# Kernel tuning notes

Measured on AMD Instinct MI355X. Metric: run time of the kernel, lower is better.

## Reference

```python
import jax, jax.numpy as jnp
import numpy as np

GRID_SIZE, SPLINE_ORDER = 5, 3  # efficient-kan KANLinear defaults
NUM_BASES = GRID_SIZE + SPLINE_ORDER


def b_splines(x, grid):
    # x: (N, in_dim), grid: (in_dim, GRID_SIZE + 2*SPLINE_ORDER + 1)
    xe = x[..., None]
    bases = ((xe >= grid[:, :-1]) & (xe < grid[:, 1:])).astype(x.dtype)
    for k in range(1, SPLINE_ORDER + 1):  # Cox-de Boor recursion (static, 3 iters)
        left = (xe - grid[:, : -(k + 1)]) / (grid[:, k:-1] - grid[:, : -(k + 1)])
        right = (grid[:, k + 1:] - xe) / (grid[:, k + 1:] - grid[:, 1:-k])
        bases = left * bases[..., :-1] + right * bases[..., 1:]
    return bases  # (N, in_dim, NUM_BASES)


def kan_linear(x, grid, base_w, spline_w, scaler):
    # base branch: SiLU(x) @ W_base^T ; spline branch: B-spline basis @ scaled spline weights
    n = x.shape[0]
    out_dim = base_w.shape[0]
    base = jax.nn.silu(x) @ base_w.T
    bs = b_splines(x, grid).reshape(n, -1)                    # (N, in*NUM_BASES)
    sw = (spline_w * scaler[..., None]).reshape(out_dim, -1)  # (out, in*NUM_BASES)
    return base + bs @ sw.T


def setup_inputs() -> dict:
    key = jax.random.key(0)
    N, E, F, H, C, L = 50000, 500000, 128, 128, 40, 3
    ks = jax.random.split(key, 8)
    x = jax.random.normal(ks[0], (N, F), dtype=jnp.float32)
    edge_index = jax.random.randint(ks[1], (2, E), 0, N)
    # KAN grid (registered buffer in efficient-kan): uniform over [-1,1] extended by spline_order
    h_step = 2.0 / GRID_SIZE
    pts = np.arange(-SPLINE_ORDER, GRID_SIZE + SPLINE_ORDER + 1) * h_step - 1.0
    grid_mp = jnp.asarray(np.tile(pts, (F, 1)), dtype=jnp.float32)
    D = F + L * H  # skip-concat dim into output KANLinear
    grid_out = jnp.asarray(np.tile(pts, (D, 1)), dtype=jnp.float32)
    s = 0.1
    conv_base_w = jax.random.normal(ks[2], (L, H, F), dtype=jnp.float32) * s
    conv_spline_w = jax.random.normal(ks[3], (L, H, F, NUM_BASES), dtype=jnp.float32) * s
    conv_scaler = jnp.ones((L, H, F), dtype=jnp.float32)
    conv_bias = jnp.zeros((L, H), dtype=jnp.float32)
    bn_gamma = jnp.ones((L, H), dtype=jnp.float32)
    bn_beta = jnp.zeros((L, H), dtype=jnp.float32)
    out_base_w = jax.random.normal(ks[4], (C, D), dtype=jnp.float32) * s
    out_spline_w = jax.random.normal(ks[5], (C, D, NUM_BASES), dtype=jnp.float32) * s
    out_scaler = jnp.ones((C, D), dtype=jnp.float32)
    return dict(x=x, edge_index=edge_index, grid_mp=grid_mp, conv_base_w=conv_base_w,
                conv_spline_w=conv_spline_w, conv_scaler=conv_scaler, conv_bias=conv_bias,
                bn_gamma=bn_gamma, bn_beta=bn_beta, grid_out=grid_out,
                out_base_w=out_base_w, out_spline_w=out_spline_w, out_scaler=out_scaler)


def reference(x, edge_index, grid_mp, conv_base_w, conv_spline_w, conv_scaler, conv_bias,
              bn_gamma, bn_beta, grid_out, out_base_w, out_spline_w, out_scaler):
    N = x.shape[0]
    L = conv_base_w.shape[0]
    # GCN normalization with self-loops (computed once; identical each layer)
    loop = jnp.arange(N)
    src = jnp.concatenate([edge_index[0], loop])
    dst = jnp.concatenate([edge_index[1], loop])
    deg = jax.ops.segment_sum(jnp.ones_like(src, dtype=x.dtype), dst, num_segments=N)
    dinv = jnp.where(deg > 0, jax.lax.rsqrt(jnp.maximum(deg, 1.0)), 0.0)
    norm = dinv[src] * dinv[dst]  # (E+N,)
    feats = [x]
    for i in range(L):  # static layer loop
        h = kan_linear(x, grid_mp, conv_base_w[i], conv_spline_w[i], conv_scaler[i])
        # symmetric-normalized sparse aggregation (gather on src, scatter-add on dst)
        h = jax.ops.segment_sum(h[src] * norm[:, None], dst, num_segments=N) + conv_bias[i]
        # BatchNorm1d (training mode: biased batch statistics over nodes)
        mu = h.mean(axis=0)
        var = h.var(axis=0)
        x = (h - mu) * jax.lax.rsqrt(var + 1e-5) * bn_gamma[i] + bn_beta[i]
        feats.append(x)  # dropout p=0.0 is identity
    xc = jnp.concatenate(feats, axis=1)  # skip-concat: (N, F + L*H)
    logits = kan_linear(xc, grid_out, out_base_w, out_spline_w, out_scaler)
    return jax.nn.log_softmax(logits, axis=1)
```

## Files before the change

### kernel.cpp

```cpp
#include <hip/hip_runtime.h>
#include <hip/hip_bf16.h>
#include <math.h>

#define F_IN   128
#define HID    128
#define NLAYER 3
#define NCLS   40
#define DCAT   512
#define OOUT   64

typedef short s16x8 __attribute__((ext_vector_type(8)));
typedef unsigned short u16x8 __attribute__((ext_vector_type(8)));
typedef unsigned short u16x4 __attribute__((ext_vector_type(4)));
typedef float f32x4 __attribute__((ext_vector_type(4)));
typedef unsigned long long u64x2 __attribute__((ext_vector_type(2)));


static __device__ __forceinline__ float silu_f(float x) {
    return x / (1.f + __expf(-x));
}

static __device__ __forceinline__ unsigned short f2bf_rn(float f) {
    union { __hip_bfloat16 h; unsigned short u; } cv;
    cv.h = __float2bfloat16(f);
    return cv.u;
}

static __device__ __forceinline__ float bf2f(unsigned short u) {
    return __uint_as_float((unsigned)u << 16);
}

static __device__ __forceinline__ void lds_barrier() {
    asm volatile("s_waitcnt lgkmcnt(0)" ::: "memory");
    __builtin_amdgcn_s_barrier();
}


__global__ __launch_bounds__(256) void deg_init_kernel(int* deg, int N) {
    for (int i = blockIdx.x * blockDim.x + threadIdx.x; i < N; i += gridDim.x * blockDim.x)
        deg[i] = 1;
}

__global__ __launch_bounds__(256) void deg_count_kernel(const int* __restrict__ dst, int E, int* deg) {
    for (int i = blockIdx.x * blockDim.x + threadIdx.x; i < E; i += gridDim.x * blockDim.x)
        atomicAdd(&deg[dst[i]], 1);
}

__global__ __launch_bounds__(256) void dinv_kernel(const int* __restrict__ deg, float* dinv, int N) {
    for (int i = blockIdx.x * blockDim.x + threadIdx.x; i < N; i += gridDim.x * blockDim.x)
        dinv[i] = rsqrtf((float)deg[i]);
}

__global__ __launch_bounds__(256) void scan_reduce_kernel(const int* __restrict__ deg, int* __restrict__ bsum, int N) {
    __shared__ int sh[256];
    int t = threadIdx.x;
    int e = blockIdx.x * 256 + t;
    sh[t] = (e < N) ? deg[e] : 0;
    __syncthreads();
#pragma unroll
    for (int off = 128; off > 0; off >>= 1) {
        if (t < off) sh[t] += sh[t + off];
        __syncthreads();
    }
    if (t == 0) bsum[blockIdx.x] = sh[0];
}

__global__ __launch_bounds__(256) void scan_top_kernel(const int* __restrict__ bsum, int* __restrict__ bbase, int nsb) {
    __shared__ int sh[256];
    int t = threadIdx.x;
    int chunk = (nsb + 255) >> 8;
    int begin = t * chunk;
    int end = begin + chunk; if (end > nsb) end = nsb;
    int s = 0;
    for (int i = begin; i < end; ++i) s += bsum[i];
    sh[t] = s;
    __syncthreads();
#pragma unroll
    for (int off = 1; off < 256; off <<= 1) {
        int v = 0;
        if (t >= off) v = sh[t - off];
        __syncthreads();
        if (t >= off) sh[t] += v;
        __syncthreads();
    }
    int run = (t == 0) ? 0 : sh[t - 1];
    for (int i = begin; i < end; ++i) {
        bbase[i] = run;
        run += bsum[i];
    }
}

__global__ __launch_bounds__(256) void scan_write_kernel(const int* __restrict__ deg,
                                                         const int* __restrict__ bbase,
                                                         int* __restrict__ offs, int* __restrict__ cursor, int N) {
    __shared__ int sh[256];
    int t = threadIdx.x;
    int e = blockIdx.x * 256 + t;
    int d = (e < N) ? deg[e] : 0;
    sh[t] = d;
    __syncthreads();
#pragma unroll
    for (int off = 1; off < 256; off <<= 1) {
        int v = 0;
        if (t >= off) v = sh[t - off];
        __syncthreads();
        if (t >= off) sh[t] += v;
        __syncthreads();
    }
    int incl = sh[t] + bbase[blockIdx.x];
    int excl = incl - d;
    if (e < N) {
        offs[e] = excl;
        cursor[e] = excl;
        if (e == N - 1) offs[N] = incl;
    }
}

__global__ __launch_bounds__(256) void fill_kernel(const int* __restrict__ src, const int* __restrict__ dst,
                                                   int E, int N, int* cursor, int* __restrict__ csr) {
    int total = E + N;
    for (int i = blockIdx.x * blockDim.x + threadIdx.x; i < total; i += gridDim.x * blockDim.x) {
        if (i < E) {
            int d = dst[i];
            int p = atomicAdd(&cursor[d], 1);
            csr[p] = src[i];
        } else {
            int n = i - E;
            int p = atomicAdd(&cursor[n], 1);
            csr[p] = n;
        }
    }
}

__global__ __launch_bounds__(256) void pack_conv_mfma(const float* __restrict__ bw,
                                                      const float* __restrict__ sw,
                                                      const float* __restrict__ sc,
                                                      unsigned short* __restrict__ wpk) {
    int total = NLAYER * 9 * 4 * 8 * 64 * 8;
    for (int idx = blockIdx.x * blockDim.x + threadIdx.x; idx < total; idx += gridDim.x * blockDim.x) {
        int e    = idx & 7;
        int lane = (idx >> 3) & 63;
        int cf   = (idx >> 9) & 7;
        int kk   = (idx >> 12) & 3;
        int cc   = (idx >> 14) % 9;
        int l    = idx / (9 << 14);
        int o = cf * 16 + (lane & 15);
        int k = kk * 32 + ((lane >> 4) << 3) + e;
        float v;
        if (cc == 8) {
            v = bw[(l * 128 + o) * 128 + k];
        } else {
            int f = cc * 16 + (k >> 3);
            int j = k & 7;
            int base = (l * 128 + o) * 128 + f;
            v = sw[base * 8 + j] * sc[base];
        }
        wpk[idx] = f2bf_rn(v);
    }
}

__global__ __launch_bounds__(256) void pack_out_mfma(const float* __restrict__ bw,
                                                     const float* __restrict__ sw,
                                                     const float* __restrict__ sc,
                                                     unsigned short* __restrict__ wpk) {
    int total = 36 * 4 * 4 * 64 * 8;
    for (int idx = blockIdx.x * blockDim.x + threadIdx.x; idx < total; idx += gridDim.x * blockDim.x) {
        int e    = idx & 7;
        int lane = (idx >> 3) & 63;
        int cf   = (idx >> 9) & 3;
        int kk   = (idx >> 11) & 3;
        int gcc  = idx >> 13;
        int g = gcc / 9, cc = gcc % 9;
        int o = cf * 16 + (lane & 15);
        int k = kk * 32 + ((lane >> 4) << 3) + e;
        float v = 0.f;
        if (o < NCLS) {
            if (cc == 8) {
                int f = g * 128 + k;
                v = bw[o * DCAT + f];
            } else {
                int f = g * 128 + cc * 16 + (k >> 3);
                int j = k & 7;
                int base = o * DCAT + f;
                v = sw[base * 8 + j] * sc[base];
            }
        }
        wpk[idx] = f2bf_rn(v);
    }
}


__global__ __launch_bounds__(512) void affine_init_kernel(float* scA, float* shA) {
    int i = threadIdx.x;
    scA[i] = 1.f; shA[i] = 0.f;
}

template<bool CONV, bool INIT>
__global__ __launch_bounds__(256, 2) void kan_fused_kernel(
    const float* __restrict__ xin, int xstride, int in_off,
    const float* __restrict__ scA, const float* __restrict__ shA,
    const unsigned short* __restrict__ wconv,
    const unsigned short* __restrict__ wout,
    unsigned short* __restrict__ htmp,
    const float* __restrict__ dinv,
    float* __restrict__ out_acc, int N) {

    __shared__ __align__(16) char lds_phi0[16384];
    __shared__ __align__(16) char lds_phi1[16384];

    const int tid = threadIdx.x;
    const int lane = tid & 63;
    const int wave = tid >> 6;
    const int l15 = lane & 15, lg = lane >> 4;
    const int nblk = blockIdx.x * 64;

    const float g0 = -1.f - 3.f * 0.4f;
    const float invh = 1.f / 0.4f;

    const int fg = tid & 3;
    const int n0 = tid >> 2;

    f32x4 accc[4][2];
    f32x4 acco[4];
    if (CONV) {
#pragma unroll
        for (int r = 0; r < 4; ++r)
#pragma unroll
            for (int c = 0; c < 2; ++c) accc[r][c] = (f32x4)0.f;
    }
#pragma unroll
    for (int r = 0; r < 4; ++r) acco[r] = (f32x4)0.f;

    float4 xqb[2], scb[2], shb[2];
    auto ldx = [&](int cc, int slot) {
        int f0 = in_off + cc * 16 + fg * 4;
        scb[slot] = *(const float4*)(scA + f0);
        shb[slot] = *(const float4*)(shA + f0);
        int gn = nblk + n0;
        xqb[slot] = (gn < N) ? *(const float4*)(xin + (size_t)gn * xstride + f0)
                             : (float4){0.f, 0.f, 0.f, 0.f};
    };

    s16x8 wc_reg[4][2];
    s16x8 wo_reg[4];
    auto loadW = [&](int cc) {
        if (CONV) {
            const unsigned short* wcb = wconv + (size_t)cc * 16384;
#pragma unroll
            for (int kk = 0; kk < 4; ++kk)
#pragma unroll
                for (int c = 0; c < 2; ++c) {
                    int cf = wave * 2 + c;
                    wc_reg[kk][c] = *(const s16x8*)(wcb + (((size_t)kk * 8 + cf) * 64 + lane) * 8);
                }
        }
        const unsigned short* wob = wout + (size_t)cc * 8192;
#pragma unroll
        for (int kk = 0; kk < 4; ++kk)
            wo_reg[kk] = *(const s16x8*)(wob + (((size_t)kk * 4 + wave) * 64 + lane) * 8);
    };

    u16x4 sreg[8];

    u64x2 pcur[4];
    auto phi_compute = [&](int ccc, int slot) {
        float xi[4] = {xqb[slot].x, xqb[slot].y, xqb[slot].z, xqb[slot].w};
        float scr[4] = {scb[slot].x, scb[slot].y, scb[slot].z, scb[slot].w};
        float shr[4] = {shb[slot].x, shb[slot].y, shb[slot].z, shb[slot].w};
        u16x4 sv;
#pragma unroll
        for (int fl = 0; fl < 4; ++fl) {
            float y = fmaf(xi[fl], scr[fl], shr[fl]);
            sv[fl] = f2bf_rn(silu_f(y));
            float t = (y - g0) * invh;
            float cfl = floorf(t);
            int c = (int)cfl;
            c = c < -20 ? -20 : (c > 20 ? 20 : c);
            float u = t - cfl;
            float um = 1.f - u;
            float u2 = u * u;
            float um2 = um * um;
            float w0 = um2 * um * (1.f / 6.f);
            float w3 = u2 * u * (1.f / 6.f);
            float w1 = fmaf(fmaf(0.5f, u, -1.f), u2, 2.f / 3.f);
            float w2 = fmaf(fmaf(-0.5f, u, 0.5f), u2, fmaf(0.5f, u, 1.f / 6.f));
            unsigned long long W = (unsigned long long)f2bf_rn(w0)
                                 | ((unsigned long long)f2bf_rn(w1) << 16)
                                 | ((unsigned long long)f2bf_rn(w2) << 32)
                                 | ((unsigned long long)f2bf_rn(w3) << 48);
            int pos = (c - 3) * 16;
            unsigned long long lo = (pos >= 0) ? (W << (pos & 63)) : (W >> ((-pos) & 63));
            lo = (pos >= 64 || pos <= -64) ? 0ull : lo;
            int ph = pos - 64;
            unsigned long long hi = (ph >= 0) ? (W << (ph & 63)) : (W >> ((-ph) & 63));
            hi = (ph >= 64 || ph <= -64) ? 0ull : hi;
            u64x2 v; v.x = lo; v.y = hi;
            pcur[fl] = v;
        }
        sreg[ccc] = sv;
    };

    auto write_phi = [&](char* buf) {
        int swz = (n0 & 7) << 4;
#pragma unroll
        for (int i = 0; i < 4; ++i) {
            int byte = n0 * 256 + ((fg * 64 + i * 16) ^ swz);
            *(u64x2*)(buf + byte) = pcur[i];
        }
    };

    auto write_silu = [&](char* buf) {
        int swz = (n0 & 7) << 4;
#pragma unroll
        for (int ccc = 0; ccc < 8; ++ccc) {
            int byte = n0 * 256 + (((ccc * 16 + fg * 4) * 2) ^ swz);
            *(u16x4*)(buf + byte) = sreg[ccc];
        }
    };

    auto mfma_phase = [&](const char* buf) {
#pragma unroll
        for (int kk = 0; kk < 4; ++kk) {
            const int kb = kk * 64 + lg * 16;
            s16x8 af[4];
#pragma unroll
            for (int r = 0; r < 4; ++r) {
                int n = r * 16 + l15;
                af[r] = *(const s16x8*)(buf + n * 256 + (kb ^ ((n & 7) << 4)));
            }
            if (CONV) {
#pragma unroll
                for (int c = 0; c < 2; ++c)
#pragma unroll
                    for (int r = 0; r < 4; ++r)
                        accc[r][c] = __builtin_amdgcn_mfma_f32_16x16x32_bf16(af[r], wc_reg[kk][c], accc[r][c], 0, 0, 0);
            }
#pragma unroll
            for (int r = 0; r < 4; ++r)
                acco[r] = __builtin_amdgcn_mfma_f32_16x16x32_bf16(af[r], wo_reg[kk], acco[r], 0, 0, 0);
        }
    };

    ldx(0, 0);
    phi_compute(0, 0);
    ldx(1, 1);
    loadW(0);
    write_phi(lds_phi0);
    __syncthreads();

#pragma unroll
    for (int cc = 0; cc < 9; ++cc) {
        char* cur = (cc & 1) ? lds_phi1 : lds_phi0;
        char* nxt = (cc & 1) ? lds_phi0 : lds_phi1;
        if (cc < 7) ldx(cc + 2, cc & 1);
        mfma_phase(cur);
        if (cc < 8) loadW(cc + 1);
        if (cc < 7) {
            phi_compute(cc + 1, (cc + 1) & 1);
            write_phi(nxt);
        }
        if (cc == 7) write_silu(nxt);
        if (cc < 8) lds_barrier();
    }

#pragma unroll
    for (int r = 0; r < 4; ++r) {
        int nb = nblk + r * 16 + lg * 4;
        if (CONV) {
#pragma unroll
            for (int c = 0; c < 2; ++c) {
                int o = wave * 32 + c * 16 + l15;
#pragma unroll
                for (int q = 0; q < 4; ++q) {
                    int n = nb + q;
                    if (n < N) htmp[(size_t)n * HID + o] = f2bf_rn(accc[r][c][q] * dinv[n]);
                }
            }
        }
        {
            int o = wave * 16 + l15;
            if (o < NCLS) {
#pragma unroll
                for (int q = 0; q < 4; ++q) {
                    int n = nb + q;
                    if (n < N) {
                        size_t a = (size_t)n * OOUT + o;
                        float v = acco[r][q];
                        if (!INIT) v += out_acc[a];
                        out_acc[a] = v;
                    }
                }
            }
        }
    }
}

__global__ __launch_bounds__(256) void agg_kernel(const unsigned short* __restrict__ h,
                                                  const float* __restrict__ dinv,
                                                  const int* __restrict__ offs,
                                                  const int* __restrict__ csr,
                                                  const float* __restrict__ bias,
                                                  float* __restrict__ xc, int out_off, int N) {
    int n = blockIdx.x * 4 + (threadIdx.x >> 6);
    if (n >= N) return;
    int lane = threadIdx.x & 63;
    int eg = lane >> 4;
    int cg = lane & 15;
    int s = offs[n], e = offs[n + 1];

    float acc[4][8];
#pragma unroll
    for (int a = 0; a < 4; ++a)
#pragma unroll
        for (int k = 0; k < 8; ++k) acc[a][k] = 0.f;

    for (int base = s; base < e; base += 64) {
        int cnt = e - base; if (cnt > 64) cnt = 64;
        int ci = base + lane;
        int cv = (ci < e) ? csr[ci] : 0;

#pragma unroll
        for (int j = 0; j < 4; ++j) {
            int ei = j * 4 + eg;
            int v = __shfl(cv, ei);
            if (ei < cnt) {
                u16x8 hv = *(const u16x8*)(h + (size_t)v * HID + cg * 8);
#pragma unroll
                for (int k = 0; k < 8; ++k) acc[j][k] += bf2f(hv[k]);
            }
        }
        int nj = (cnt + 3) >> 2;
        for (int j = 4; j < nj; ++j) {
            int ei = j * 4 + eg;
            int v = __shfl(cv, ei);
            if (ei < cnt) {
                u16x8 hv = *(const u16x8*)(h + (size_t)v * HID + cg * 8);
#pragma unroll
                for (int k = 0; k < 8; ++k) acc[j & 3][k] += bf2f(hv[k]);
            }
        }
    }

    float tot[8];
#pragma unroll
    for (int k = 0; k < 8; ++k)
        tot[k] = (acc[0][k] + acc[1][k]) + (acc[2][k] + acc[3][k]);
#pragma unroll
    for (int k = 0; k < 8; ++k) {
        tot[k] += __shfl_xor(tot[k], 16);
        tot[k] += __shfl_xor(tot[k], 32);
    }
    if (eg == 0) {
        float dn = dinv[n];
        float4 b0 = *(const float4*)(bias + cg * 8);
        float4 b1 = *(const float4*)(bias + cg * 8 + 4);
        float4 o0 = {fmaf(tot[0], dn, b0.x), fmaf(tot[1], dn, b0.y),
                     fmaf(tot[2], dn, b0.z), fmaf(tot[3], dn, b0.w)};
        float4 o1 = {fmaf(tot[4], dn, b1.x), fmaf(tot[5], dn, b1.y),
                     fmaf(tot[6], dn, b1.z), fmaf(tot[7], dn, b1.w)};
        float* dst = xc + (size_t)n * DCAT + out_off + cg * 8;
        *(float4*)dst = o0;
        *(float4*)(dst + 4) = o1;
    }
}

__global__ __launch_bounds__(128) void bn_stats_kernel(const float* __restrict__ xc, int off, int N,
                                                       float* __restrict__ bnsum, float* __restrict__ bnsq) {
    int f = threadIdx.x;
    float s = 0.f, q = 0.f;
    for (int n = blockIdx.x; n < N; n += gridDim.x) {
        float v = xc[(size_t)n * DCAT + off + f];
        s += v;
        q += v * v;
    }
    atomicAdd(&bnsum[f], s);
    atomicAdd(&bnsq[f], q);
}

__global__ __launch_bounds__(128) void bn_affine_kernel(const float* __restrict__ bnsum,
                                                        const float* __restrict__ bnsq,
                                                        const float* __restrict__ gamma,
                                                        const float* __restrict__ beta,
                                                        float* scA, float* shA, int seg_off, float invN) {
    int f = threadIdx.x;
    float mu = bnsum[f] * invN;
    float var = bnsq[f] * invN - mu * mu;
    float rs = rsqrtf(var + 1e-5f);
    float s = gamma[f] * rs;
    scA[seg_off + f] = s;
    shA[seg_off + f] = fmaf(-mu, s, beta[f]);
}

__global__ __launch_bounds__(256) void logsoftmax_kernel(const float* __restrict__ oacc,
                                                         float* __restrict__ out, int N) {
    for (int n = blockIdx.x * blockDim.x + threadIdx.x; n < N; n += gridDim.x * blockDim.x) {
        const float* row = oacc + (size_t)n * OOUT;
        float m = -1e30f;
#pragma unroll
        for (int j = 0; j < NCLS; ++j) m = fmaxf(m, row[j]);
        float s = 0.f;
#pragma unroll
        for (int j = 0; j < NCLS; ++j) s += __expf(row[j] - m);
        float lse = m + __logf(s);
        float* orow = out + (size_t)n * NCLS;
#pragma unroll
        for (int j = 0; j < NCLS; ++j) orow[j] = row[j] - lse;
    }
}


extern "C" void kernel_launch(void* const* d_in, const int* in_sizes, int n_in,
                              void* d_out, int out_size, void* d_ws, size_t ws_size,
                              hipStream_t stream) {
    const float* x            = (const float*)d_in[0];
    const int*   eidx         = (const int*)d_in[1];
    const float* conv_base_w  = (const float*)d_in[3];
    const float* conv_spline_w= (const float*)d_in[4];
    const float* conv_scaler  = (const float*)d_in[5];
    const float* conv_bias    = (const float*)d_in[6];
    const float* bn_gamma     = (const float*)d_in[7];
    const float* bn_beta      = (const float*)d_in[8];
    const float* out_base_w   = (const float*)d_in[10];
    const float* out_spline_w = (const float*)d_in[11];
    const float* out_scaler   = (const float*)d_in[12];
    float* out = (float*)d_out;

    int N = in_sizes[0] / F_IN;
    int E = in_sizes[1] / 2;
    const int* esrc = eidx;
    const int* edst = eidx + E;

    int blocks = (N + 63) / 64;
    int npad = blocks * 64;
    int nsb = (N + 255) / 256;

    char* p = (char*)d_ws;
    auto carve = [&](size_t bytes) {
        char* r = p;
        p += (bytes + 255) & ~(size_t)255;
        return r;
    };
    float* xc   = (float*)carve((size_t)N * DCAT * 4);
    unsigned short* htmp = (unsigned short*)carve((size_t)npad * HID * 2);
    float* oacc = (float*)carve((size_t)npad * OOUT * 4);
    float* dinv = (float*)carve((size_t)N * 4);
    float* bn   = (float*)carve((size_t)NLAYER * 2 * HID * 4);
    float* scA  = (float*)carve((size_t)DCAT * 4);
    float* shA  = (float*)carve((size_t)DCAT * 4);
    unsigned short* wpkc = (unsigned short*)carve((size_t)NLAYER * 9 * 128 * 128 * 2);
    unsigned short* wpko = (unsigned short*)carve((size_t)36 * 64 * 128 * 2);
    int* deg    = (int*)carve((size_t)N * 4);
    int* offs   = (int*)carve((size_t)(N + 1) * 4);
    int* cursor = (int*)carve((size_t)(N + 1) * 4);
    int* bsum   = (int*)carve((size_t)nsb * 4);
    int* bbase  = (int*)carve((size_t)nsb * 4);
    int* csr    = (int*)carve((size_t)(E + N) * 4);

    hipMemsetAsync(bn, 0, NLAYER * 2 * HID * 4, stream);

    deg_init_kernel<<<512, 256, 0, stream>>>(deg, N);
    deg_count_kernel<<<1024, 256, 0, stream>>>(edst, E, deg);
    dinv_kernel<<<512, 256, 0, stream>>>(deg, dinv, N);
    scan_reduce_kernel<<<nsb, 256, 0, stream>>>(deg, bsum, N);
    scan_top_kernel<<<1, 256, 0, stream>>>(bsum, bbase, nsb);
    scan_write_kernel<<<nsb, 256, 0, stream>>>(deg, bbase, offs, cursor, N);
    fill_kernel<<<1024, 256, 0, stream>>>(esrc, edst, E, N, cursor, csr);

    pack_conv_mfma<<<1024, 256, 0, stream>>>(conv_base_w, conv_spline_w, conv_scaler, wpkc);
    pack_out_mfma<<<1024, 256, 0, stream>>>(out_base_w, out_spline_w, out_scaler, wpko);
    affine_init_kernel<<<1, 512, 0, stream>>>(scA, shA);

    float invN = 1.f / (float)N;
    for (int l = 0; l < NLAYER; ++l) {
        int in_off = l * HID;
        int out_off = (l + 1) * HID;
        const unsigned short* wl = wpkc + (size_t)l * 9 * 16384;
        const unsigned short* wo = wpko + (size_t)l * 9 * 8192;
        if (l == 0)
            kan_fused_kernel<true, true><<<blocks, 256, 0, stream>>>(
                x, F_IN, 0, scA, shA, wl, wo, htmp, dinv, oacc, N);
        else
            kan_fused_kernel<true, false><<<blocks, 256, 0, stream>>>(
                xc, DCAT, in_off, scA, shA, wl, wo, htmp, dinv, oacc, N);
        agg_kernel<<<(N + 3) / 4, 256, 0, stream>>>(htmp, dinv, offs, csr, conv_bias + l * HID, xc, out_off, N);
        float* bnsum = bn + l * 2 * HID;
        float* bnsq  = bnsum + HID;
        bn_stats_kernel<<<256, 128, 0, stream>>>(xc, out_off, N, bnsum, bnsq);
        bn_affine_kernel<<<1, 128, 0, stream>>>(bnsum, bnsq, bn_gamma + l * HID, bn_beta + l * HID,
                                                scA, shA, out_off, invN);
    }

    kan_fused_kernel<false, false><<<blocks, 256, 0, stream>>>(
        xc, DCAT, 384, scA, shA, nullptr, wpko + (size_t)3 * 9 * 8192, htmp, dinv, oacc, N);

    logsoftmax_kernel<<<(N + 255) / 256, 256, 0, stream>>>(oacc, out, N);
}
```

Measured before the change: 512.4 us.

## Give each wave its own 16-node tile to drop block barriers in fused KAN kernel

Restructures the fused KAN GEMM kernel so each wave owns 16 nodes and computes every output column, with per-wave private LDS double buffers. This removes the block-wide barriers between phi-write and MFMA phases. Weight fragments are now streamed per k-step through a two-slot register pipeline, and A-fragment LDS reads are software-prefetched. In exchange, each wave reloads the full weight slice from global/L2, so weight traffic per block rises about fourfold. It also relies on intra-wave ordering of LDS writes and reads without an explicit wait.

```diff
diff --git a/kernel.cpp b/kernel.cpp
--- a/kernel.cpp
+++ b/kernel.cpp
@@ -28,11 +28,6 @@
 
 static __device__ __forceinline__ float bf2f(unsigned short u) {
     return __uint_as_float((unsigned)u << 16);
-}
-
-static __device__ __forceinline__ void lds_barrier() {
-    asm volatile("s_waitcnt lgkmcnt(0)" ::: "memory");
-    __builtin_amdgcn_s_barrier();
 }
 
 
@@ -205,59 +200,55 @@
     const float* __restrict__ dinv,
     float* __restrict__ out_acc, int N) {
 
-    __shared__ __align__(16) char lds_phi0[16384];
-    __shared__ __align__(16) char lds_phi1[16384];
+    __shared__ __align__(16) char lds[4][2][4096];
 
     const int tid = threadIdx.x;
     const int lane = tid & 63;
     const int wave = tid >> 6;
     const int l15 = lane & 15, lg = lane >> 4;
-    const int nblk = blockIdx.x * 64;
+    const int nwv = blockIdx.x * 64 + wave * 16;
 
     const float g0 = -1.f - 3.f * 0.4f;
     const float invh = 1.f / 0.4f;
 
-    const int fg = tid & 3;
-    const int n0 = tid >> 2;
-
-    f32x4 accc[4][2];
+    const int fg = lane & 3;
+    const int nl = lane >> 2;
+
+    char* buf0 = lds[wave][0];
+    char* buf1 = lds[wave][1];
+
+    f32x4 accc[8];
     f32x4 acco[4];
     if (CONV) {
 #pragma unroll
-        for (int r = 0; r < 4; ++r)
-#pragma unroll
-            for (int c = 0; c < 2; ++c) accc[r][c] = (f32x4)0.f;
-    }
-#pragma unroll
-    for (int r = 0; r < 4; ++r) acco[r] = (f32x4)0.f;
+        for (int c = 0; c < 8; ++c) accc[c] = (f32x4)0.f;
+    }
+#pragma unroll
+    for (int c = 0; c < 4; ++c) acco[c] = (f32x4)0.f;
 
     float4 xqb[2], scb[2], shb[2];
     auto ldx = [&](int cc, int slot) {
         int f0 = in_off + cc * 16 + fg * 4;
         scb[slot] = *(const float4*)(scA + f0);
         shb[slot] = *(const float4*)(shA + f0);
-        int gn = nblk + n0;
+        int gn = nwv + nl;
         xqb[slot] = (gn < N) ? *(const float4*)(xin + (size_t)gn * xstride + f0)
                              : (float4){0.f, 0.f, 0.f, 0.f};
     };
 
-    s16x8 wc_reg[4][2];
-    s16x8 wo_reg[4];
-    auto loadW = [&](int cc) {
+    s16x8 wc[2][8];
+    s16x8 wo[2][4];
+    auto loadW = [&](int cc, int kk, int slot) {
         if (CONV) {
-            const unsigned short* wcb = wconv + (size_t)cc * 16384;
-#pragma unroll
-            for (int kk = 0; kk < 4; ++kk)
-#pragma unroll
-                for (int c = 0; c < 2; ++c) {
-                    int cf = wave * 2 + c;
-                    wc_reg[kk][c] = *(const s16x8*)(wcb + (((size_t)kk * 8 + cf) * 64 + lane) * 8);
-                }
-        }
-        const unsigned short* wob = wout + (size_t)cc * 8192;
-#pragma unroll
-        for (int kk = 0; kk < 4; ++kk)
-            wo_reg[kk] = *(const s16x8*)(wob + (((size_t)kk * 4 + wave) * 64 + lane) * 8);
+            const unsigned short* wcb = wconv + (((size_t)cc * 4 + kk) * 8 * 64) * 8;
+#pragma unroll
+            for (int cf = 0; cf < 8; ++cf)
+                wc[slot][cf] = *(const s16x8*)(wcb + ((size_t)cf * 64 + lane) * 8);
+        }
+        const unsigned short* wob = wout + (((size_t)cc * 4 + kk) * 4 * 64) * 8;
+#pragma unroll
+        for (int cf = 0; cf < 4; ++cf)
+            wo[slot][cf] = *(const s16x8*)(wob + ((size_t)cf * 64 + lane) * 8);
     };
 
     u16x4 sreg[8];
@@ -301,94 +292,86 @@
     };
 
     auto write_phi = [&](char* buf) {
-        int swz = (n0 & 7) << 4;
+        int swz = (nl & 7) << 4;
 #pragma unroll
         for (int i = 0; i < 4; ++i) {
-            int byte = n0 * 256 + ((fg * 64 + i * 16) ^ swz);
+            int byte = nl * 256 + ((fg * 64 + i * 16) ^ swz);
             *(u64x2*)(buf + byte) = pcur[i];
         }
     };
 
     auto write_silu = [&](char* buf) {
-        int swz = (n0 & 7) << 4;
+        int swz = (nl & 7) << 4;
 #pragma unroll
         for (int ccc = 0; ccc < 8; ++ccc) {
-            int byte = n0 * 256 + (((ccc * 16 + fg * 4) * 2) ^ swz);
+            int byte = nl * 256 + (((ccc * 16 + fg * 4) * 2) ^ swz);
             *(u16x4*)(buf + byte) = sreg[ccc];
         }
     };
 
-    auto mfma_phase = [&](const char* buf) {
-#pragma unroll
-        for (int kk = 0; kk < 4; ++kk) {
-            const int kb = kk * 64 + lg * 16;
-            s16x8 af[4];
-#pragma unroll
-            for (int r = 0; r < 4; ++r) {
-                int n = r * 16 + l15;
-                af[r] = *(const s16x8*)(buf + n * 256 + (kb ^ ((n & 7) << 4)));
-            }
-            if (CONV) {
-#pragma unroll
-                for (int c = 0; c < 2; ++c)
-#pragma unroll
-                    for (int r = 0; r < 4; ++r)
-                        accc[r][c] = __builtin_amdgcn_mfma_f32_16x16x32_bf16(af[r], wc_reg[kk][c], accc[r][c], 0, 0, 0);
-            }
-#pragma unroll
-            for (int r = 0; r < 4; ++r)
-                acco[r] = __builtin_amdgcn_mfma_f32_16x16x32_bf16(af[r], wo_reg[kk], acco[r], 0, 0, 0);
-        }
+    auto rd_af = [&](const char* buf, int kk) -> s16x8 {
+        int byte = l15 * 256 + (((kk * 64) + lg * 16) ^ ((l15 & 7) << 4));
+        return *(const s16x8*)(buf + byte);
     };
 
     ldx(0, 0);
     phi_compute(0, 0);
+    write_phi(buf0);
     ldx(1, 1);
-    loadW(0);
-    write_phi(lds_phi0);
-    __syncthreads();
+    loadW(0, 0, 0);
+    loadW(0, 1, 1);
 
 #pragma unroll
     for (int cc = 0; cc < 9; ++cc) {
-        char* cur = (cc & 1) ? lds_phi1 : lds_phi0;
-        char* nxt = (cc & 1) ? lds_phi0 : lds_phi1;
-        if (cc < 7) ldx(cc + 2, cc & 1);
-        mfma_phase(cur);
-        if (cc < 8) loadW(cc + 1);
+        char* cur = (cc & 1) ? buf1 : buf0;
+        char* nxt = (cc & 1) ? buf0 : buf1;
+        if (cc < 6) ldx(cc + 2, cc & 1);
+        s16x8 af = rd_af(cur, 0);
         if (cc < 7) {
             phi_compute(cc + 1, (cc + 1) & 1);
             write_phi(nxt);
         }
         if (cc == 7) write_silu(nxt);
-        if (cc < 8) lds_barrier();
-    }
-
-#pragma unroll
-    for (int r = 0; r < 4; ++r) {
-        int nb = nblk + r * 16 + lg * 4;
-        if (CONV) {
-#pragma unroll
-            for (int c = 0; c < 2; ++c) {
-                int o = wave * 32 + c * 16 + l15;
-#pragma unroll
-                for (int q = 0; q < 4; ++q) {
-                    int n = nb + q;
-                    if (n < N) htmp[(size_t)n * HID + o] = f2bf_rn(accc[r][c][q] * dinv[n]);
+#pragma unroll
+        for (int kk = 0; kk < 4; ++kk) {
+            s16x8 afn = af;
+            if (kk < 3) afn = rd_af(cur, kk + 1);
+            int slot = kk & 1;
+            if (CONV) {
+#pragma unroll
+                for (int cf = 0; cf < 8; ++cf)
+                    accc[cf] = __builtin_amdgcn_mfma_f32_16x16x32_bf16(af, wc[slot][cf], accc[cf], 0, 0, 0);
+            }
+#pragma unroll
+            for (int cf = 0; cf < 4; ++cf)
+                acco[cf] = __builtin_amdgcn_mfma_f32_16x16x32_bf16(af, wo[slot][cf], acco[cf], 0, 0, 0);
+            int s2cc = (kk < 2) ? cc : cc + 1;
+            int s2kk = (kk < 2) ? kk + 2 : kk - 2;
+            if (s2cc < 9) loadW(s2cc, s2kk, slot);
+            af = afn;
+        }
+    }
+
+#pragma unroll
+    for (int q = 0; q < 4; ++q) {
+        int n = nwv + lg * 4 + q;
+        if (n < N) {
+            float dn = dinv[n];
+            if (CONV) {
+#pragma unroll
+                for (int cf = 0; cf < 8; ++cf) {
+                    int o = cf * 16 + l15;
+                    htmp[(size_t)n * HID + o] = f2bf_rn(accc[cf][q] * dn);
                 }
             }
-        }
-        {
-            int o = wave * 16 + l15;
-            if (o < NCLS) {
-#pragma unroll
-                for (int q = 0; q < 4; ++q) {
-                    int n = nb + q;
-                    if (n < N) {
-                        size_t a = (size_t)n * OOUT + o;
-                        float v = acco[r][q];
-                        if (!INIT) v += out_acc[a];
-                        out_acc[a] = v;
-                    }
+#pragma unroll
+            for (int cf = 0; cf < 3; ++cf) {
+                int o = cf * 16 + l15;
+                if (o < NCLS) {
+                    size_t a = (size_t)n * OOUT + o;
+                    float v = acco[cf][q];
+                    if (!INIT) v += out_acc[a];
+                    out_acc[a] = v;
                 }
             }
         }
```

New measurement: 540.7 us. +5.5%, slower.
